# Kernel optimization log

Measured on AMD Instinct MI355X. Metric: run time of the kernel, lower is better.

Reference implementation:

```python
import jax, jax.numpy as jnp
import numpy as np

P, D_IN, RANK, D_OUT, N = 64, 1024, 64, 1024, 4096


def setup_inputs() -> dict:
    key = jax.random.key(0)
    k1, k2, k3, k4, k5 = jax.random.split(key, 5)
    x = jax.random.normal(k1, (N, D_IN), dtype=jnp.float32)
    pids = jax.random.randint(k2, (N,), 0, P, dtype=jnp.int64)
    U = jax.random.normal(k3, (P, D_IN, RANK), dtype=jnp.float32) * 0.02
    V = jax.random.normal(k4, (P, RANK, D_OUT), dtype=jnp.float32) * 0.02
    bias = jax.random.normal(k5, (D_OUT,), dtype=jnp.float32)
    return {"x": x, "pids": pids, "U": U, "V": V, "bias": bias}


def reference(x, pids, U, V, bias):
    # Equivalent to: for each token n, out[n] = x[n] @ U[pids[n]] @ V[pids[n]] + bias
    # Computed as dense grouped GEMM over all partitions, then row-select by pid
    # (identical math to the masked per-partition loop in the torch module).
    h = jnp.einsum('nd,pdr->pnr', x, U)        # [P, N, R]
    o = jnp.einsum('pnr,pro->pno', h, V)       # [P, N, D_out]
    out = o[pids, jnp.arange(x.shape[0])] + bias  # select each token's own partition
    return out
```

## Files before the change

kernel.cpp:

```cpp
#include <hip/hip_runtime.h>
#include <hip/hip_bf16.h>

#define NP     64
#define D_IN   1024
#define RANK   64
#define D_OUT  1024
#define NTOK   4096
#define TM     64
#define BK     64
#define MT     128
#define KS     8
#define KW     (D_IN / KS)
#define OW     128
#define LDSTR  72

typedef __bf16 bf16x8 __attribute__((ext_vector_type(8)));
typedef float  f32x4  __attribute__((ext_vector_type(4)));

__device__ __forceinline__ unsigned short f2bf(float f) {
    unsigned u = __builtin_bit_cast(unsigned, f);
    u += 0x7FFFu + ((u >> 16) & 1u);
    return (unsigned short)(u >> 16);
}
__device__ __forceinline__ float bf2f(unsigned short s) {
    unsigned u = (unsigned)s << 16;
    return __builtin_bit_cast(float, u);
}
__device__ __forceinline__ bf16x8 pack8(float4 a, float4 b) {
    union { bf16x8 v; unsigned short s[8]; } r;
    r.s[0] = f2bf(a.x); r.s[1] = f2bf(a.y); r.s[2] = f2bf(a.z); r.s[3] = f2bf(a.w);
    r.s[4] = f2bf(b.x); r.s[5] = f2bf(b.y); r.s[6] = f2bf(b.z); r.s[7] = f2bf(b.w);
    return r.v;
}

__global__ void bucket_kernel(const int* __restrict__ pids, int* __restrict__ meta) {
    __shared__ int counts[NP];
    __shared__ int cursor[NP];
    int tid = threadIdx.x;
    if (tid < NP) counts[tid] = 0;
    __syncthreads();
    for (int i = tid; i < NTOK; i += 256)
        atomicAdd(&counts[pids[i] & (NP - 1)], 1);
    __syncthreads();
    if (tid < 64) {
        int c = counts[tid];
        int ntp = (c + TM - 1) >> 6;
        int sc = c, st = ntp;
        for (int d = 1; d < 64; d <<= 1) {
            int vc = __shfl_up(sc, d);
            int vt = __shfl_up(st, d);
            if (tid >= d) { sc += vc; st += vt; }
        }
        int cbase = sc - c;
        int tb    = st - ntp;
        cursor[tid] = cbase;
        for (int t = 0; t < ntp; ++t) {
            int idx = tb + t;
            meta[16 + idx]  = tid;
            meta[144 + idx] = cbase + t * TM;
            int rem = c - t * TM;
            meta[272 + idx] = rem < TM ? rem : TM;
        }
        if (tid == 63) meta[0] = st;
    }
    __syncthreads();
    int* bucket = meta + 512;
    for (int i = tid; i < NTOK; i += 256) {
        int p = pids[i] & (NP - 1);
        int pos = atomicAdd(&cursor[p], 1);
        bucket[pos] = i;
    }
}

__global__ __launch_bounds__(256, 4) void h_kernel(
    const float* __restrict__ x, const float* __restrict__ U,
    const int* __restrict__ meta, unsigned short* __restrict__ Hpart)
{
    __shared__ __align__(16) unsigned short Us[2][RANK][LDSTR];
    __shared__ int toks[TM];

    int tile = blockIdx.x >> 3;
    int ks   = blockIdx.x & 7;
    int nt = meta[0];
    if (tile >= nt) return;
    int p   = meta[16 + tile];
    int off = meta[144 + tile];
    int len = meta[272 + tile];

    int tid  = threadIdx.x;
    int lane = tid & 63;
    int w    = tid >> 6;
    int l15  = lane & 15;
    int l4   = lane >> 4;

    const int* bucket = meta + 512;
    if (tid < TM) toks[tid] = (tid < len) ? bucket[off + tid] : -1;
    __syncthreads();

    int myrow = w * 16 + l15;
    int t = toks[myrow];
    bool valid = (t >= 0);
    const float* xrow = x + (size_t)(valid ? t : 0) * D_IN;
    const float* Up = U + (size_t)p * D_IN * RANK;

    int kbeg = ks * KW;
    int kk = tid >> 2;
    int q  = (tid & 3) * 16;

    float4 z{0,0,0,0};
    float4 c0a=z,c0b=z,c0c=z,c0d=z,c1a=z,c1b=z,c1c=z,c1d=z;
    if (valid) {
        const float* xp = xrow + kbeg + l4 * 8;
        c0a = *reinterpret_cast<const float4*>(xp);
        c0b = *reinterpret_cast<const float4*>(xp + 4);
        c0c = *reinterpret_cast<const float4*>(xp + 32);
        c0d = *reinterpret_cast<const float4*>(xp + 36);
        c1a = *reinterpret_cast<const float4*>(xp + 64);
        c1b = *reinterpret_cast<const float4*>(xp + 68);
        c1c = *reinterpret_cast<const float4*>(xp + 96);
        c1d = *reinterpret_cast<const float4*>(xp + 100);
    }

    f32x4 acc[4] = {};

    {
        const float* up = Up + (size_t)(kbeg + kk) * RANK + q;
#pragma unroll
        for (int i = 0; i < 4; ++i) {
            float4 v = *reinterpret_cast<const float4*>(up + i * 4);
            int r = q + i * 4;
            Us[0][r + 0][kk] = f2bf(v.x);
            Us[0][r + 1][kk] = f2bf(v.y);
            Us[0][r + 2][kk] = f2bf(v.z);
            Us[0][r + 3][kk] = f2bf(v.w);
        }
    }
    __syncthreads();

    float4 u10, u11, u12, u13;
    {
        const float* up = Up + (size_t)(kbeg + BK + kk) * RANK + q;
        u10 = *reinterpret_cast<const float4*>(up);
        u11 = *reinterpret_cast<const float4*>(up + 4);
        u12 = *reinterpret_cast<const float4*>(up + 8);
        u13 = *reinterpret_cast<const float4*>(up + 12);
    }

    {
        bf16x8 a0 = pack8(c0a, c0b);
        bf16x8 a1 = pack8(c0c, c0d);
#pragma unroll
        for (int k2 = 0; k2 < 2; ++k2) {
            int kof = k2 * 32 + l4 * 8;
            bf16x8 a = k2 ? a1 : a0;
#pragma unroll
            for (int ni = 0; ni < 4; ++ni) {
                bf16x8 b = *reinterpret_cast<const bf16x8*>(&Us[0][ni * 16 + l15][kof]);
                acc[ni] = __builtin_amdgcn_mfma_f32_16x16x32_bf16(a, b, acc[ni], 0, 0, 0);
            }
        }
    }

    {
        float4 vv[4] = {u10, u11, u12, u13};
#pragma unroll
        for (int i = 0; i < 4; ++i) {
            int r = q + i * 4;
            Us[1][r + 0][kk] = f2bf(vv[i].x);
            Us[1][r + 1][kk] = f2bf(vv[i].y);
            Us[1][r + 2][kk] = f2bf(vv[i].z);
            Us[1][r + 3][kk] = f2bf(vv[i].w);
        }
    }
    __syncthreads();

    {
        bf16x8 a0 = pack8(c1a, c1b);
        bf16x8 a1 = pack8(c1c, c1d);
#pragma unroll
        for (int k2 = 0; k2 < 2; ++k2) {
            int kof = k2 * 32 + l4 * 8;
            bf16x8 a = k2 ? a1 : a0;
#pragma unroll
            for (int ni = 0; ni < 4; ++ni) {
                bf16x8 b = *reinterpret_cast<const bf16x8*>(&Us[1][ni * 16 + l15][kof]);
                acc[ni] = __builtin_amdgcn_mfma_f32_16x16x32_bf16(a, b, acc[ni], 0, 0, 0);
            }
        }
    }

    unsigned short* hp = Hpart + ((size_t)ks * MT + tile) * (TM * RANK);
#pragma unroll
    for (int ni = 0; ni < 4; ++ni)
#pragma unroll
        for (int j = 0; j < 4; ++j) {
            int row = w * 16 + l4 * 4 + j;
            int col = ni * 16 + l15;
            hp[row * RANK + col] = f2bf(acc[ni][j]);
        }
}

__global__ __launch_bounds__(256, 4) void o_kernel(
    const float* __restrict__ V, const float* __restrict__ bias,
    const int* __restrict__ meta, const unsigned short* __restrict__ Hpart,
    float* __restrict__ out)
{
    __shared__ __align__(16) unsigned short Vs[OW][LDSTR];
    __shared__ int toks[TM];

    int tile = blockIdx.x >> 3;
    int oc   = (blockIdx.x & 7) * OW;
    int nt = meta[0];
    if (tile >= nt) return;
    int p   = meta[16 + tile];
    int off = meta[144 + tile];
    int len = meta[272 + tile];

    int tid  = threadIdx.x;
    int lane = tid & 63;
    int w    = tid >> 6;
    int l15  = lane & 15;
    int l4   = lane >> 4;

    const int* bucket = meta + 512;
    if (tid < TM) toks[tid] = (tid < len) ? bucket[off + tid] : -1;

    const float* Vp = V + (size_t)p * RANK * D_OUT;
    int o4 = (tid & 31) * 4;
    int rb = tid >> 5;
    float4 vv[8];
#pragma unroll
    for (int pass = 0; pass < 8; ++pass) {
        int r = pass * 8 + rb;
        vv[pass] = *reinterpret_cast<const float4*>(&Vp[(size_t)r * D_OUT + oc + o4]);
    }

    size_t hoff = (size_t)tile * (TM * RANK) + (w * 16 + l15) * RANK + l4 * 8;
    float s0[8] = {}, s1[8] = {};
#pragma unroll
    for (int k = 0; k < KS; ++k) {
        const unsigned short* pp = Hpart + (size_t)k * (MT * TM * RANK) + hoff;
        union { int4 i4; unsigned short u[8]; } va, vb;
        va.i4 = *reinterpret_cast<const int4*>(pp);
        vb.i4 = *reinterpret_cast<const int4*>(pp + 32);
#pragma unroll
        for (int j = 0; j < 8; ++j) { s0[j] += bf2f(va.u[j]); s1[j] += bf2f(vb.u[j]); }
    }
    union { bf16x8 v; unsigned short u[8]; } fa0, fa1;
#pragma unroll
    for (int j = 0; j < 8; ++j) { fa0.u[j] = f2bf(s0[j]); fa1.u[j] = f2bf(s1[j]); }

#pragma unroll
    for (int pass = 0; pass < 8; ++pass) {
        int r = pass * 8 + rb;
        Vs[o4 + 0][r] = f2bf(vv[pass].x);
        Vs[o4 + 1][r] = f2bf(vv[pass].y);
        Vs[o4 + 2][r] = f2bf(vv[pass].z);
        Vs[o4 + 3][r] = f2bf(vv[pass].w);
    }
    __syncthreads();

    f32x4 acc[8] = {};
#pragma unroll
    for (int k2 = 0; k2 < 2; ++k2) {
        int kof = k2 * 32 + l4 * 8;
        bf16x8 a = k2 ? fa1.v : fa0.v;
#pragma unroll
        for (int ni = 0; ni < 8; ++ni) {
            bf16x8 b = *reinterpret_cast<const bf16x8*>(&Vs[ni * 16 + l15][kof]);
            acc[ni] = __builtin_amdgcn_mfma_f32_16x16x32_bf16(a, b, acc[ni], 0, 0, 0);
        }
    }

    int r0 = w * 16 + l4 * 4;
    int t0 = toks[r0 + 0], t1 = toks[r0 + 1], t2 = toks[r0 + 2], t3 = toks[r0 + 3];
#pragma unroll
    for (int ni = 0; ni < 8; ++ni) {
        int col = oc + ni * 16 + l15;
        float bv = bias[col];
        if (r0 + 0 < len) out[(size_t)t0 * D_OUT + col] = acc[ni][0] + bv;
        if (r0 + 1 < len) out[(size_t)t1 * D_OUT + col] = acc[ni][1] + bv;
        if (r0 + 2 < len) out[(size_t)t2 * D_OUT + col] = acc[ni][2] + bv;
        if (r0 + 3 < len) out[(size_t)t3 * D_OUT + col] = acc[ni][3] + bv;
    }
}

extern "C" void kernel_launch(void* const* d_in, const int* in_sizes, int n_in,
                              void* d_out, int out_size, void* d_ws, size_t ws_size,
                              hipStream_t stream) {
    const float* x    = (const float*)d_in[0];
    const int*   pids = (const int*)d_in[1];
    const float* U    = (const float*)d_in[2];
    const float* V    = (const float*)d_in[3];
    const float* bias = (const float*)d_in[4];
    float* out = (float*)d_out;

    int* meta = (int*)d_ws;
    unsigned short* Hpart = (unsigned short*)((char*)d_ws + 65536);

    bucket_kernel<<<1, 256, 0, stream>>>(pids, meta);
    h_kernel<<<MT * KS, 256, 0, stream>>>(x, U, meta, Hpart);
    o_kernel<<<MT * 8, 256, 0, stream>>>(V, bias, meta, Hpart, out);
}
```

Measured before the change: 44.90 us.

## Swizzle LDS tiles, remap blocks across XCDs, pack tile metadata, vectorize bucketing

```diff
diff --git a/kernel.cpp b/kernel.cpp
--- a/kernel.cpp
+++ b/kernel.cpp
@@ -33,14 +33,32 @@
     return r.v;
 }
 
+__device__ __forceinline__ int swz_idx(int outer, int inner) {
+    int blk = (inner >> 3) ^ ((outer >> 3) & 7);
+    return outer * LDSTR + blk * 8 + (inner & 7);
+}
+
+__device__ __forceinline__ void decode_xcd(int b, int& tile, int& slice) {
+    int g = b & 7;
+    int l = b >> 3;
+    slice = l >> 4;
+    int m = l & 15;
+    tile = (((m >> 1) << 3) | g) * 2 + (m & 1);
+}
+
 __global__ void bucket_kernel(const int* __restrict__ pids, int* __restrict__ meta) {
     __shared__ int counts[NP];
     __shared__ int cursor[NP];
     int tid = threadIdx.x;
     if (tid < NP) counts[tid] = 0;
     __syncthreads();
-    for (int i = tid; i < NTOK; i += 256)
-        atomicAdd(&counts[pids[i] & (NP - 1)], 1);
+    for (int i = tid; i < NTOK / 4; i += 256) {
+        int4 pv = reinterpret_cast<const int4*>(pids)[i];
+        atomicAdd(&counts[pv.x & (NP - 1)], 1);
+        atomicAdd(&counts[pv.y & (NP - 1)], 1);
+        atomicAdd(&counts[pv.z & (NP - 1)], 1);
+        atomicAdd(&counts[pv.w & (NP - 1)], 1);
+    }
     __syncthreads();
     if (tid < 64) {
         int c = counts[tid];
@@ -56,19 +74,20 @@
         cursor[tid] = cbase;
         for (int t = 0; t < ntp; ++t) {
             int idx = tb + t;
-            meta[16 + idx]  = tid;
-            meta[144 + idx] = cbase + t * TM;
             int rem = c - t * TM;
-            meta[272 + idx] = rem < TM ? rem : TM;
+            int4 rec = {tid, cbase + t * TM, rem < TM ? rem : TM, 0};
+            *reinterpret_cast<int4*>(meta + 16 + 4 * idx) = rec;
         }
         if (tid == 63) meta[0] = st;
     }
     __syncthreads();
-    int* bucket = meta + 512;
-    for (int i = tid; i < NTOK; i += 256) {
-        int p = pids[i] & (NP - 1);
-        int pos = atomicAdd(&cursor[p], 1);
-        bucket[pos] = i;
+    int* bucket = meta + 1024;
+    for (int i = tid; i < NTOK / 4; i += 256) {
+        int4 pv = reinterpret_cast<const int4*>(pids)[i];
+        bucket[atomicAdd(&cursor[pv.x & (NP - 1)], 1)] = i * 4 + 0;
+        bucket[atomicAdd(&cursor[pv.y & (NP - 1)], 1)] = i * 4 + 1;
+        bucket[atomicAdd(&cursor[pv.z & (NP - 1)], 1)] = i * 4 + 2;
+        bucket[atomicAdd(&cursor[pv.w & (NP - 1)], 1)] = i * 4 + 3;
     }
 }
 
@@ -76,16 +95,15 @@
     const float* __restrict__ x, const float* __restrict__ U,
     const int* __restrict__ meta, unsigned short* __restrict__ Hpart)
 {
-    __shared__ __align__(16) unsigned short Us[2][RANK][LDSTR];
+    __shared__ __align__(16) unsigned short Us[2][RANK * LDSTR];
     __shared__ int toks[TM];
 
-    int tile = blockIdx.x >> 3;
-    int ks   = blockIdx.x & 7;
+    int tile, ks;
+    decode_xcd(blockIdx.x, tile, ks);
     int nt = meta[0];
     if (tile >= nt) return;
-    int p   = meta[16 + tile];
-    int off = meta[144 + tile];
-    int len = meta[272 + tile];
+    int4 ti = *reinterpret_cast<const int4*>(meta + 16 + 4 * tile);
+    int p = ti.x, off = ti.y, len = ti.z;
 
     int tid  = threadIdx.x;
     int lane = tid & 63;
@@ -93,7 +111,7 @@
     int l15  = lane & 15;
     int l4   = lane >> 4;
 
-    const int* bucket = meta + 512;
+    const int* bucket = meta + 1024;
     if (tid < TM) toks[tid] = (tid < len) ? bucket[off + tid] : -1;
     __syncthreads();
 
@@ -129,10 +147,10 @@
         for (int i = 0; i < 4; ++i) {
             float4 v = *reinterpret_cast<const float4*>(up + i * 4);
             int r = q + i * 4;
-            Us[0][r + 0][kk] = f2bf(v.x);
-            Us[0][r + 1][kk] = f2bf(v.y);
-            Us[0][r + 2][kk] = f2bf(v.z);
-            Us[0][r + 3][kk] = f2bf(v.w);
+            Us[0][swz_idx(r + 0, kk)] = f2bf(v.x);
+            Us[0][swz_idx(r + 1, kk)] = f2bf(v.y);
+            Us[0][swz_idx(r + 2, kk)] = f2bf(v.z);
+            Us[0][swz_idx(r + 3, kk)] = f2bf(v.w);
         }
     }
     __syncthreads();
@@ -155,7 +173,7 @@
             bf16x8 a = k2 ? a1 : a0;
 #pragma unroll
             for (int ni = 0; ni < 4; ++ni) {
-                bf16x8 b = *reinterpret_cast<const bf16x8*>(&Us[0][ni * 16 + l15][kof]);
+                bf16x8 b = *reinterpret_cast<const bf16x8*>(&Us[0][swz_idx(ni * 16 + l15, kof)]);
                 acc[ni] = __builtin_amdgcn_mfma_f32_16x16x32_bf16(a, b, acc[ni], 0, 0, 0);
             }
         }
@@ -166,10 +184,10 @@
 #pragma unroll
         for (int i = 0; i < 4; ++i) {
             int r = q + i * 4;
-            Us[1][r + 0][kk] = f2bf(vv[i].x);
-            Us[1][r + 1][kk] = f2bf(vv[i].y);
-            Us[1][r + 2][kk] = f2bf(vv[i].z);
-            Us[1][r + 3][kk] = f2bf(vv[i].w);
+            Us[1][swz_idx(r + 0, kk)] = f2bf(vv[i].x);
+            Us[1][swz_idx(r + 1, kk)] = f2bf(vv[i].y);
+            Us[1][swz_idx(r + 2, kk)] = f2bf(vv[i].z);
+            Us[1][swz_idx(r + 3, kk)] = f2bf(vv[i].w);
         }
     }
     __syncthreads();
@@ -183,7 +201,7 @@
             bf16x8 a = k2 ? a1 : a0;
 #pragma unroll
             for (int ni = 0; ni < 4; ++ni) {
-                bf16x8 b = *reinterpret_cast<const bf16x8*>(&Us[1][ni * 16 + l15][kof]);
+                bf16x8 b = *reinterpret_cast<const bf16x8*>(&Us[1][swz_idx(ni * 16 + l15, kof)]);
                 acc[ni] = __builtin_amdgcn_mfma_f32_16x16x32_bf16(a, b, acc[ni], 0, 0, 0);
             }
         }
@@ -205,16 +223,16 @@
     const int* __restrict__ meta, const unsigned short* __restrict__ Hpart,
     float* __restrict__ out)
 {
-    __shared__ __align__(16) unsigned short Vs[OW][LDSTR];
+    __shared__ __align__(16) unsigned short Vs[OW * LDSTR];
     __shared__ int toks[TM];
 
-    int tile = blockIdx.x >> 3;
-    int oc   = (blockIdx.x & 7) * OW;
+    int tile, ocs;
+    decode_xcd(blockIdx.x, tile, ocs);
+    int oc = ocs * OW;
     int nt = meta[0];
     if (tile >= nt) return;
-    int p   = meta[16 + tile];
-    int off = meta[144 + tile];
-    int len = meta[272 + tile];
+    int4 ti = *reinterpret_cast<const int4*>(meta + 16 + 4 * tile);
+    int p = ti.x, off = ti.y, len = ti.z;
 
     int tid  = threadIdx.x;
     int lane = tid & 63;
@@ -222,7 +240,7 @@
     int l15  = lane & 15;
     int l4   = lane >> 4;
 
-    const int* bucket = meta + 512;
+    const int* bucket = meta + 1024;
     if (tid < TM) toks[tid] = (tid < len) ? bucket[off + tid] : -1;
 
     const float* Vp = V + (size_t)p * RANK * D_OUT;
@@ -253,10 +271,10 @@
 #pragma unroll
     for (int pass = 0; pass < 8; ++pass) {
         int r = pass * 8 + rb;
-        Vs[o4 + 0][r] = f2bf(vv[pass].x);
-        Vs[o4 + 1][r] = f2bf(vv[pass].y);
-        Vs[o4 + 2][r] = f2bf(vv[pass].z);
-        Vs[o4 + 3][r] = f2bf(vv[pass].w);
+        Vs[swz_idx(o4 + 0, r)] = f2bf(vv[pass].x);
+        Vs[swz_idx(o4 + 1, r)] = f2bf(vv[pass].y);
+        Vs[swz_idx(o4 + 2, r)] = f2bf(vv[pass].z);
+        Vs[swz_idx(o4 + 3, r)] = f2bf(vv[pass].w);
     }
     __syncthreads();
 
@@ -267,7 +285,7 @@
         bf16x8 a = k2 ? fa1.v : fa0.v;
 #pragma unroll
         for (int ni = 0; ni < 8; ++ni) {
-            bf16x8 b = *reinterpret_cast<const bf16x8*>(&Vs[ni * 16 + l15][kof]);
+            bf16x8 b = *reinterpret_cast<const bf16x8*>(&Vs[swz_idx(ni * 16 + l15, kof)]);
             acc[ni] = __builtin_amdgcn_mfma_f32_16x16x32_bf16(a, b, acc[ni], 0, 0, 0);
         }
     }
```

Result: faster. 37.74 us (-15.9%).
